# Kernel optimization log

Measured on AMD Instinct MI355X. Metric: run time of the kernel, lower is better.

Reference implementation:

```python
import jax, jax.numpy as jnp
import numpy as np

WS = 8          # window_size
NH = 8          # num_heads
IQKV = 128      # inner_qk_v_dim
IQKC = 32       # inner_qk_c_dim
IVV = 64        # inner_v_v_dim
EPS = 1e-6
B, HH, WW, DV, DC = 2, 224, 224, 256, 64


def _rmsnorm(x, g):
    return x * jax.lax.rsqrt(jnp.mean(x * x, axis=-1, keepdims=True) + EPS) * g


def _window(x):
    # (b, h, w, d) -> (b, Wh, Ww, ws*ws, d)
    b, h, w, d = x.shape
    x = x.reshape(b, h // WS, WS, w // WS, WS, d).transpose(0, 1, 3, 2, 4, 5)
    return x.reshape(b, h // WS, w // WS, WS * WS, d)


def _unwindow(x, h, w):
    # (b, N, ws*ws, d) -> (b, h, w, d)
    b, _, _, d = x.shape
    x = x.reshape(b, h // WS, w // WS, WS, WS, d).transpose(0, 1, 3, 2, 4, 5)
    return x.reshape(b, h, w, d)


def _source_qkv(V, C, Wqk_v, bqk_v, g_v, Wqk_c, bqk_c, g_c, Wv):
    Vw, Cw = _window(V), _window(C)          # (b, Wh, Ww, n, d)
    b, Wh, Ww, n, _ = Vw.shape
    N = Wh * Ww
    Vavg, Cavg = Vw.mean(-2), Cw.mean(-2)
    qk_v = _rmsnorm(Vavg @ Wqk_v + bqk_v, g_v)   # (b, Wh, Ww, 2*IQKV)
    qk_c = _rmsnorm(Cavg @ Wqk_c + bqk_c, g_c)   # (b, Wh, Ww, 2*IQKC)
    # 'b Wh Ww (H e) -> b H (Wh Ww) e' then chunk2 along e
    qk_v = qk_v.reshape(b, N, NH, -1).transpose(0, 2, 1, 3)
    qk_c = qk_c.reshape(b, N, NH, -1).transpose(0, 2, 1, 3)
    ev, ec = qk_v.shape[-1] // 2, qk_c.shape[-1] // 2
    qv, kv = qk_v[..., :ev], qk_v[..., ev:]
    qc, kc = qk_c[..., :ec], qk_c[..., ec:]
    # value projection: 'b Wh Ww n (e H) -> b H (Wh Ww) (n e)'
    e = IVV // NH
    Vv = (Vw @ Wv).reshape(b, N, n, e, NH).transpose(0, 4, 1, 2, 3).reshape(b, NH, N, n * e)
    return qv, kv, qc, kc, Vv, (Wh, Ww)


def _forward(values0, coords0, values1, coords1,
             Wqk_v, bqk_v, g_v, Wqk_c, bqk_c, g_c, Wv, Wback):
    parts = [_source_qkv(V, C, Wqk_v, bqk_v, g_v, Wqk_c, bqk_c, g_c, Wv)
             for V, C in ((values0, coords0), (values1, coords1))]
    qv = jnp.concatenate([p[0] for p in parts], axis=2)
    kv = jnp.concatenate([p[1] for p in parts], axis=2)
    qc = jnp.concatenate([p[2] for p in parts], axis=2)
    kc = jnp.concatenate([p[3] for p in parts], axis=2)
    Vv = jnp.concatenate([p[4] for p in parts], axis=2)
    scores = (jnp.einsum('bhqe,bhke->bhqk', qv, kv) / jnp.sqrt(jnp.float32(IQKV))
              + jnp.einsum('bhqe,bhke->bhqk', qc, kc) / jnp.sqrt(jnp.float32(IQKC)))
    A = jax.nn.softmax(scores, axis=-1)            # (b, H, N, N)
    rw = jnp.einsum('bhqk,bhkf->bhqf', A, Vv)      # (b, H, N, n*e)
    b, _, N, _ = rw.shape
    n, e = WS * WS, IVV // NH
    # 'b H N (n e) -> b N n (e H)'
    rw = rw.reshape(b, NH, N, n, e).transpose(0, 2, 3, 4, 1).reshape(b, N, n, e * NH)
    rw = rw @ Wback                                # (b, N, n, Dv)
    outs, off = [], 0
    for (V, _), p in zip(((values0, coords0), (values1, coords1)), parts):
        Wh, Ww = p[5]
        Ns = Wh * Ww
        outs.append(_unwindow(rw[:, off:off + Ns], Wh * WS, Ww * WS))
        off += Ns
    return tuple(outs)


def setup_inputs() -> dict:
    key = jax.random.key(0)
    ks = jax.random.split(key, 8)
    s = 0.02
    return {
        'values0': jax.random.normal(ks[0], (B, HH, WW, DV), jnp.float32),
        'coords0': jax.random.normal(ks[1], (B, HH, WW, DC), jnp.float32),
        'values1': jax.random.normal(ks[2], (B, HH, WW, DV), jnp.float32),
        'coords1': jax.random.normal(ks[3], (B, HH, WW, DC), jnp.float32),
        'Wqk_v': s * jax.random.normal(ks[4], (DV, 2 * IQKV), jnp.float32),
        'bqk_v': jnp.zeros((2 * IQKV,), jnp.float32),
        'g_v': jnp.ones((2 * IQKV,), jnp.float32),
        'Wqk_c': s * jax.random.normal(ks[5], (DC, 2 * IQKC), jnp.float32),
        'bqk_c': jnp.zeros((2 * IQKC,), jnp.float32),
        'g_c': jnp.ones((2 * IQKC,), jnp.float32),
        'Wv': s * jax.random.normal(ks[6], (DV, IVV), jnp.float32),
        'Wback': s * jax.random.normal(ks[7], (IVV, DV), jnp.float32),
    }


def reference(values0, coords0, values1, coords1,
              Wqk_v, bqk_v, g_v, Wqk_c, bqk_c, g_c, Wv, Wback):
    return _forward(values0, coords0, values1, coords1,
                    Wqk_v, bqk_v, g_v, Wqk_c, bqk_c, g_c, Wv, Wback)
```

## Files before the change

### kernel.cpp

```cpp
#include <hip/hip_runtime.h>

#define NSRC 784
#define NTOT 1568
#define NHD 8
#define DVC 256
#define DCC 64
#define D20 20
#define FDIM 512
#define OUT_PER_SRC 25690112

typedef short s16x8 __attribute__((ext_vector_type(8)));
typedef unsigned short u16x8 __attribute__((ext_vector_type(8)));
typedef float f32x4 __attribute__((ext_vector_type(4)));
typedef float f32x16 __attribute__((ext_vector_type(16)));
typedef unsigned u32x4 __attribute__((ext_vector_type(4)));

__device__ __forceinline__ unsigned short f2bf(float x) {
    unsigned u = __float_as_uint(x);
    unsigned r = (u + 0x7FFFu + ((u >> 16) & 1u)) >> 16;
    return (unsigned short)r;
}

__device__ __forceinline__ unsigned cvt_pk_bf16(float lo, float hi) {
    unsigned r;
    asm volatile("v_cvt_pk_bf16_f32 %0, %1, %2" : "=v"(r) : "v"(lo), "v"(hi));
    return r;
}

__device__ __forceinline__ void split_bf(float x, unsigned short& hi, unsigned short& lo) {
    unsigned short h = f2bf(x);
    float hf = __uint_as_float(((unsigned)h) << 16);
    hi = h;
    lo = f2bf(x - hf);
}

__global__ __launch_bounds__(256) void kz_zero(unsigned short* __restrict__ p) {
    size_t i = (size_t)blockIdx.x * 256 + threadIdx.x;
    u16x8 z = (u16x8)0;
    *(u16x8*)&p[i * 8] = z;
}

__global__ __launch_bounds__(256) void k0_wsplit(
    const float* __restrict__ Wv,
    unsigned short* __restrict__ WThi, unsigned short* __restrict__ WTlo) {
    int e = blockIdx.x, dd = threadIdx.x;
    float x = Wv[dd * DCC + e];
    unsigned short h, l;
    split_bf(x, h, l);
    WThi[e * 256 + dd] = h;
    WTlo[e * 256 + dd] = l;
}

__global__ __launch_bounds__(256) void k0b_wback(
    const float* __restrict__ Wb, unsigned short* __restrict__ Wp) {
    int idx = blockIdx.x * 256 + threadIdx.x;
    int jj = idx & 7, lane = (idx >> 3) & 63, hl = (idx >> 9) & 1;
    int kc = (idx >> 10) & 1, mt = idx >> 11;
    int c = mt * 16 + (lane & 15);
    int j = kc * 32 + (lane >> 4) * 8 + jj;
    unsigned short h, l;
    split_bf(Wb[j * 256 + c], h, l);
    Wp[idx] = hl ? l : h;
}

__global__ __launch_bounds__(256) void k1c_avg(
    const float* __restrict__ c0, const float* __restrict__ c1,
    float* __restrict__ Cavg) {
    int wi = blockIdx.x * 4 + (threadIdx.x >> 6);
    int d = threadIdx.x & 63;
    int b = wi / NTOT, N = wi % NTOT;
    int src = N / NSRC, nloc = N % NSRC;
    int wh = nloc / 28, ww = nloc % 28;
    const float* __restrict__ C = src ? c1 : c0;
    int pbase = (b * 224 + wh * 8) * 224 + ww * 8;
    float s = 0.f;
#pragma unroll 8
    for (int p = 0; p < 64; ++p)
        s += C[(size_t)(pbase + (p >> 3) * 224 + (p & 7)) * DCC + d];
    Cavg[(size_t)wi * DCC + d] = s * 0.015625f;
}

__global__ __launch_bounds__(256) void k2_qk(
    const float* __restrict__ Vavg, const float* __restrict__ Cavg,
    const float* __restrict__ Wqkv, const float* __restrict__ bqkv, const float* __restrict__ gv,
    const float* __restrict__ Wqkc, const float* __restrict__ bqkc, const float* __restrict__ gc,
    unsigned short* __restrict__ Qp, unsigned short* __restrict__ Kp) {
    __shared__ float xv[DVC];
    __shared__ float xc[DCC];
    __shared__ float wred[4];
    int blk = blockIdx.x;
    int b = blk / NTOT, N = blk % NTOT;
    int t = threadIdx.x;
    int tile = N >> 5, l31 = N & 31;
    xv[t] = Vavg[(size_t)blk * DVC + t];
    if (t < DCC) xc[t] = Cavg[(size_t)blk * DCC + t];
    __syncthreads();
    float yv = bqkv[t];
#pragma unroll 4
    for (int d = 0; d < DVC; ++d) yv += xv[d] * Wqkv[d * 256 + t];
    float ss = yv * yv;
#pragma unroll
    for (int off = 32; off; off >>= 1) ss += __shfl_xor(ss, off, 64);
    if ((t & 63) == 0) wred[t >> 6] = ss;
    __syncthreads();
    float tot = wred[0] + wred[1] + wred[2] + wred[3];
    float rv = rsqrtf(tot * (1.f / 256.f) + 1e-6f);
    float yn = yv * rv * gv[t];
    int h = t >> 5, c = t & 31;
    int bh = b * NHD + h;
    {
        int isq = (c < 16);
        int d = isq ? c : c - 16;
        float val = isq ? yn * 0.088388347648318447f : yn;
        unsigned short h16, l16;
        split_bf(val, h16, l16);
        int hh = d >> 3, j = d & 7;
        size_t base = ((size_t)(bh * 49 + tile) * 4) * 512 + (size_t)(hh * 32 + l31) * 8 + j;
        unsigned short* dst = isq ? Qp : Kp;
        dst[base] = h16;
        dst[base + 1024] = l16;
    }
    if (t < DCC) {
        float yc = bqkc[t];
#pragma unroll 4
        for (int d = 0; d < DCC; ++d) yc += xc[d] * Wqkc[d * 64 + t];
        float sc = yc * yc;
#pragma unroll
        for (int off = 32; off; off >>= 1) sc += __shfl_xor(sc, off, 64);
        float rc = rsqrtf(sc * (1.f / 64.f) + 1e-6f);
        float ycn = yc * rc * gc[t];
        int h2 = t >> 3, c2 = t & 7;
        int bh2 = b * NHD + h2;
        int isq = (c2 < 4);
        int dd = isq ? c2 : c2 - 4;
        float val = isq ? ycn * 0.17677669529663687f : ycn;
        unsigned short h16, l16;
        split_bf(val, h16, l16);
        size_t base = ((size_t)(bh2 * 49 + tile) * 4 + 1) * 512 + (size_t)l31 * 8 + dd;
        unsigned short* dst = isq ? Qp : Kp;
        dst[base] = h16;
        dst[base + 1024] = l16;
    }
}

__global__ __launch_bounds__(256) void k3_vv(
    const float* __restrict__ v0, const float* __restrict__ v1,
    const unsigned short* __restrict__ WThi, const unsigned short* __restrict__ WTlo,
    unsigned short* __restrict__ Vvb, float* __restrict__ Vavg) {
    __shared__ unsigned short Ahi[64 * 40];
    __shared__ unsigned short Alo[64 * 40];
    __shared__ float avgpart[256];
    __shared__ float avgrow[256];
    int blk = blockIdx.x;
    int b = blk / NTOT, N = blk % NTOT;
    int src = N / NSRC, nloc = N % NSRC;
    int wh = nloc / 28, ww = nloc % 28;
    const float* __restrict__ V = src ? v1 : v0;
    int t = threadIdx.x;
    int w = t >> 6, lane = t & 63;
    int lm = lane & 15, lk = lane >> 4;
    int ddl = t & 31;
    int pg = t >> 5;
    int pbase = (b * 224 + wh * 8) * 224 + ww * 8;
    const float* xptr[8];
#pragma unroll
    for (int i = 0; i < 8; ++i) {
        int px = i * 8 + pg;
        xptr[i] = V + (size_t)(pbase + (px >> 3) * 224 + (px & 7)) * DVC + ddl;
    }
    f32x4 acc4[4];
#pragma unroll
    for (int nt = 0; nt < 4; ++nt) acc4[nt] = (f32x4)0.f;

    for (int c = 0; c < 8; ++c) {
        int d0 = c * 32;
        float xs[8];
#pragma unroll
        for (int i = 0; i < 8; ++i) xs[i] = xptr[i][d0];
        float part = 0.f;
#pragma unroll
        for (int i = 0; i < 8; ++i) part += xs[i];
        __syncthreads();
        avgpart[t] = part;
#pragma unroll
        for (int i = 0; i < 8; ++i) {
            int px = i * 8 + pg;
            unsigned short h, l;
            split_bf(xs[i], h, l);
            Ahi[px * 40 + ddl] = h;
            Alo[px * 40 + ddl] = l;
        }
        __syncthreads();
        if (t < 32) {
            float s = 0.f;
#pragma unroll
            for (int g = 0; g < 8; ++g) s += avgpart[g * 32 + t];
            avgrow[d0 + t] = s * 0.015625f;
        }
        s16x8 ahi = *(const s16x8*)&Ahi[(w * 16 + lm) * 40 + lk * 8];
        s16x8 alo = *(const s16x8*)&Alo[(w * 16 + lm) * 40 + lk * 8];
#pragma unroll
        for (int nt = 0; nt < 4; ++nt) {
            int e = nt * 16 + lm;
            s16x8 bhi = *(const s16x8*)&WThi[e * 256 + d0 + lk * 8];
            s16x8 blo = *(const s16x8*)&WTlo[e * 256 + d0 + lk * 8];
            acc4[nt] = __builtin_amdgcn_mfma_f32_16x16x32_bf16(ahi, blo, acc4[nt], 0, 0, 0);
            acc4[nt] = __builtin_amdgcn_mfma_f32_16x16x32_bf16(alo, bhi, acc4[nt], 0, 0, 0);
            acc4[nt] = __builtin_amdgcn_mfma_f32_16x16x32_bf16(ahi, bhi, acc4[nt], 0, 0, 0);
        }
    }
#pragma unroll
    for (int nt = 0; nt < 4; ++nt) {
        int e = nt * 16 + lm;
#pragma unroll
        for (int r = 0; r < 4; ++r) {
            int px = w * 16 + lk * 4 + r;
            Vvb[((size_t)(b * NHD + (e & 7)) * NTOT + N) * FDIM + px * 8 + (e >> 3)] = f2bf(acc4[nt][r]);
        }
    }
    __syncthreads();
    Vavg[(size_t)blk * DVC + t] = avgrow[t];
}

__global__ __launch_bounds__(256) void k3b_pack(
    const unsigned short* __restrict__ Vvb, unsigned short* __restrict__ Vp) {
    __shared__ unsigned short tile[32 * 520];
    int kt = blockIdx.x, bh = blockIdx.y;
    int t = threadIdx.x;
    const unsigned short* src = Vvb + ((size_t)bh * NTOT + kt * 32) * FDIM;
#pragma unroll
    for (int it = 0; it < 8; ++it) {
        int flat = it * 256 + t;
        int r = flat >> 6, c8 = (flat & 63) * 8;
        *(u16x8*)&tile[r * 520 + c8] = *(const u16x8*)&src[(size_t)r * FDIM + c8];
    }
    __syncthreads();
    unsigned short* dst = Vp + ((size_t)bh * 49 + kt) * 16384;
#pragma unroll
    for (int it = 0; it < 8; ++it) {
        int flato = it * 256 + t;
        int lane = flato & 63;
        int kh = (flato >> 6) & 1;
        int sub = (flato >> 7) & 3;
        int w = flato >> 9;
        int l31 = lane & 31, hh = lane >> 5;
        int f = w * 128 + sub * 32 + l31;
        int kbase = kh * 16 + hh * 8;
        u16x8 v;
#pragma unroll
        for (int j = 0; j < 8; ++j) v[j] = tile[(kbase + j) * 520 + f];
        *(u16x8*)&dst[(size_t)flato * 8] = v;
    }
}

__global__ __launch_bounds__(256) void k4_attn(
    const unsigned short* __restrict__ Qp, const unsigned short* __restrict__ Kp,
    const unsigned short* __restrict__ Vp, float* __restrict__ rw) {
    __shared__ float ebuf[32 * 132];
    int wg = blockIdx.x;
    int qt = wg >> 4, bh = wg & 15;
    int q0 = qt * 32;
    int t = threadIdx.x;
    int w = t >> 6, lane = t & 63;
    int l31 = lane & 31, hh = lane >> 5;

    const unsigned short* __restrict__ Qpb = Qp + ((size_t)(bh * 49 + qt) * 4) * 512 + lane * 8;
    const unsigned short* __restrict__ Kpb = Kp + (size_t)bh * 49 * 2048 + lane * 8;
    const unsigned short* __restrict__ Vpb = Vp + (size_t)bh * 49 * 16384 + lane * 8;

    s16x8 qa0 = *(const s16x8*)&Qpb[0];
    s16x8 qa1 = *(const s16x8*)&Qpb[512];
    s16x8 ql0 = *(const s16x8*)&Qpb[1024];
    s16x8 ql1 = *(const s16x8*)&Qpb[1536];

    s16x8 ka0 = *(const s16x8*)&Kpb[0];
    s16x8 ka1 = *(const s16x8*)&Kpb[512];
    s16x8 kl0 = *(const s16x8*)&Kpb[1024];
    s16x8 kl1 = *(const s16x8*)&Kpb[1536];

    float m = -1e30f, lsum = 0.f;
    f32x16 acc[4];
#pragma unroll
    for (int s = 0; s < 4; ++s) acc[s] = (f32x16)0.f;

    for (int kt = 0; kt < NTOT / 32; ++kt) {
        const unsigned short* Vtile = Vpb + (size_t)kt * 16384 + (w * 8) * 512;
        s16x8 va[8];
#pragma unroll
        for (int fr = 0; fr < 8; ++fr)
            va[fr] = *(const s16x8*)&Vtile[fr * 512];
        int ktn = (kt < 48) ? kt + 1 : 48;
        const unsigned short* Ktn = Kpb + (size_t)ktn * 2048;
        s16x8 kn0 = *(const s16x8*)&Ktn[0];
        s16x8 kn1 = *(const s16x8*)&Ktn[512];
        s16x8 kn2 = *(const s16x8*)&Ktn[1024];
        s16x8 kn3 = *(const s16x8*)&Ktn[1536];

        f32x16 sacc = (f32x16)0.f;
        sacc = __builtin_amdgcn_mfma_f32_32x32x16_bf16(kl0, qa0, sacc, 0, 0, 0);
        sacc = __builtin_amdgcn_mfma_f32_32x32x16_bf16(ka0, ql0, sacc, 0, 0, 0);
        sacc = __builtin_amdgcn_mfma_f32_32x32x16_bf16(ka0, qa0, sacc, 0, 0, 0);
        sacc = __builtin_amdgcn_mfma_f32_32x32x16_bf16(kl1, qa1, sacc, 0, 0, 0);
        sacc = __builtin_amdgcn_mfma_f32_32x32x16_bf16(ka1, ql1, sacc, 0, 0, 0);
        sacc = __builtin_amdgcn_mfma_f32_32x32x16_bf16(ka1, qa1, sacc, 0, 0, 0);

        float tmax = sacc[0];
#pragma unroll
        for (int r = 1; r < 16; ++r) tmax = fmaxf(tmax, sacc[r]);
        tmax = fmaxf(tmax, __shfl_xor(tmax, 32, 64));
        if (__any(tmax > m + 8.f)) {
            float mn = fmaxf(m, tmax);
            float sc = __expf(m - mn);
#pragma unroll
            for (int s = 0; s < 4; ++s) acc[s] = acc[s] * sc;
            lsum *= sc;
            m = mn;
        }
        unsigned P2[8];
        float tsum = 0.f;
#pragma unroll
        for (int j = 0; j < 8; ++j) {
            float pa = __expf(sacc[2 * j] - m);
            float pb = __expf(sacc[2 * j + 1] - m);
            tsum += pa + pb;
            P2[j] = cvt_pk_bf16(pa, pb);
        }
        lsum += tsum + __shfl_xor(tsum, 32, 64);
        unsigned X2[8];
#pragma unroll
        for (int j = 0; j < 8; ++j) X2[j] = (unsigned)__shfl_xor((int)P2[j], 32, 64);
        u32x4 b0u, b1u;
        if (hh == 0) {
            b0u[0] = P2[0]; b0u[1] = P2[1]; b0u[2] = X2[0]; b0u[3] = X2[1];
            b1u[0] = P2[4]; b1u[1] = P2[5]; b1u[2] = X2[4]; b1u[3] = X2[5];
        } else {
            b0u[0] = X2[2]; b0u[1] = X2[3]; b0u[2] = P2[2]; b0u[3] = P2[3];
            b1u[0] = X2[6]; b1u[1] = X2[7]; b1u[2] = P2[6]; b1u[3] = P2[7];
        }
        s16x8 pb0 = __builtin_bit_cast(s16x8, b0u);
        s16x8 pb1 = __builtin_bit_cast(s16x8, b1u);

#pragma unroll
        for (int sub = 0; sub < 4; ++sub) {
            acc[sub] = __builtin_amdgcn_mfma_f32_32x32x16_bf16(va[2 * sub],     pb0, acc[sub], 0, 0, 0);
            acc[sub] = __builtin_amdgcn_mfma_f32_32x32x16_bf16(va[2 * sub + 1], pb1, acc[sub], 0, 0, 0);
        }
        ka0 = kn0; ka1 = kn1; kl0 = kn2; kl1 = kn3;
    }

    float inv = 1.f / lsum;
    float* rwg = rw + ((size_t)bh * NTOT + q0) * FDIM;
#pragma unroll
    for (int c = 0; c < 4; ++c) {
        __syncthreads();
        if (w == c) {
#pragma unroll
            for (int sub = 0; sub < 4; ++sub) {
#pragma unroll
                for (int r = 0; r < 16; ++r) {
                    int fl = sub * 32 + (r & 3) + 8 * (r >> 2) + 4 * hh;
                    ebuf[l31 * 132 + fl] = acc[sub][r] * inv;
                }
            }
        }
        __syncthreads();
        int qr = t >> 3, cb = (t & 7) * 16;
#pragma unroll
        for (int j = 0; j < 4; ++j) {
            *(float4*)&rwg[(size_t)qr * FDIM + c * 128 + cb + j * 4] =
                *(const float4*)&ebuf[qr * 132 + cb + j * 4];
        }
    }
}

__global__ __launch_bounds__(256) void k5_back(
    const float* __restrict__ rw, const unsigned short* __restrict__ Wp,
    float* __restrict__ out) {
    __shared__ unsigned short SB[2 * 64 * 72];
    unsigned short* BhL = SB;
    unsigned short* BlL = SB + 64 * 72;
    int blk = blockIdx.x;
    int b = blk / NTOT, N = blk % NTOT;
    int src = N / NSRC, nloc = N % NSRC;
    int wh = nloc / 28, ww = nloc % 28;
    int t = threadIdx.x;
    int w = t >> 6, lane = t & 63;
    int lm = lane & 15, lk = lane >> 4;
    int pbase = (b * 224 + wh * 8) * 224 + ww * 8;

#pragma unroll
    for (int i = 0; i < 4; ++i) {
        int flat4 = i * 256 + t;
        int h = flat4 >> 7;
        int f0 = (flat4 & 127) * 4;
        float4 v = *(const float4*)&rw[((size_t)(b * NHD + h) * NTOT + N) * FDIM + f0];
        int n = f0 >> 3;
        int ebase = f0 & 7;
        float vv[4] = {v.x, v.y, v.z, v.w};
#pragma unroll
        for (int u = 0; u < 4; ++u) {
            int j8 = ebase + u;
            unsigned short h16, l16;
            split_bf(vv[u], h16, l16);
            int col = ((j8 ^ (n & 7)) << 3) | h;
            BhL[n * 72 + col] = h16;
            BlL[n * 72 + col] = l16;
        }
    }
    __syncthreads();

    f32x4 acc[4][4];
#pragma unroll
    for (int mi = 0; mi < 4; ++mi)
#pragma unroll
        for (int nt = 0; nt < 4; ++nt) acc[mi][nt] = (f32x4)0.f;

    const unsigned short* Wpw = Wp + (size_t)(w * 4) * 2048 + lane * 8;
#pragma unroll
    for (int kc = 0; kc < 2; ++kc) {
        s16x8 Ah[4], Al[4], Bh4[4], Bl4[4];
#pragma unroll
        for (int mi = 0; mi < 4; ++mi) {
            int base = mi * 2048 + kc * 1024;
            Ah[mi] = *(const s16x8*)&Wpw[base];
            Al[mi] = *(const s16x8*)&Wpw[base + 512];
        }
#pragma unroll
        for (int nt = 0; nt < 4; ++nt) {
            int n = nt * 16 + lm;
            int addr = n * 72 + (((kc * 4 + lk) ^ (n & 7)) << 3);
            Bh4[nt] = *(const s16x8*)&BhL[addr];
            Bl4[nt] = *(const s16x8*)&BlL[addr];
        }
#pragma unroll
        for (int mi = 0; mi < 4; ++mi)
#pragma unroll
            for (int nt = 0; nt < 4; ++nt) {
                acc[mi][nt] = __builtin_amdgcn_mfma_f32_16x16x32_bf16(Ah[mi], Bl4[nt], acc[mi][nt], 0, 0, 0);
                acc[mi][nt] = __builtin_amdgcn_mfma_f32_16x16x32_bf16(Al[mi], Bh4[nt], acc[mi][nt], 0, 0, 0);
                acc[mi][nt] = __builtin_amdgcn_mfma_f32_16x16x32_bf16(Ah[mi], Bh4[nt], acc[mi][nt], 0, 0, 0);
            }
    }

    float* eb = (float*)SB;
    float* outp = out + (size_t)src * OUT_PER_SRC;
#pragma unroll
    for (int ch = 0; ch < 4; ++ch) {
        __syncthreads();
        if (w == ch) {
#pragma unroll
            for (int mi = 0; mi < 4; ++mi)
#pragma unroll
                for (int nt = 0; nt < 4; ++nt)
#pragma unroll
                    for (int r = 0; r < 4; ++r) {
                        int n = nt * 16 + lm;
                        int cl = mi * 16 + lk * 4 + r;
                        eb[n * 68 + cl] = acc[mi][nt][r];
                    }
        }
        __syncthreads();
#pragma unroll
        for (int i = 0; i < 4; ++i) {
            int fl4 = i * 256 + t;
            int n = fl4 >> 4, c4 = (fl4 & 15) * 4;
            int opix = pbase + (n >> 3) * 224 + (n & 7);
            *(float4*)&outp[(size_t)opix * DVC + ch * 64 + c4] =
                *(const float4*)&eb[n * 68 + c4];
        }
    }
}

extern "C" void kernel_launch(void* const* d_in, const int* in_sizes, int n_in,
                              void* d_out, int out_size, void* d_ws, size_t ws_size,
                              hipStream_t stream) {
    const float* v0   = (const float*)d_in[0];
    const float* c0   = (const float*)d_in[1];
    const float* v1   = (const float*)d_in[2];
    const float* c1   = (const float*)d_in[3];
    const float* Wqkv = (const float*)d_in[4];
    const float* bqkv = (const float*)d_in[5];
    const float* gv   = (const float*)d_in[6];
    const float* Wqkc = (const float*)d_in[7];
    const float* bqkc = (const float*)d_in[8];
    const float* gc   = (const float*)d_in[9];
    const float* Wv   = (const float*)d_in[10];
    const float* Wbk  = (const float*)d_in[11];

    float* ws = (float*)d_ws;
    float* rw   = ws;
    float* Vavg = ws;
    float* Cavg = ws + 802816;
    unsigned short* Qp   = (unsigned short*)(ws + 12845056);
    unsigned short* Kp   = (unsigned short*)(ws + 13647872);
    unsigned short* WThi = (unsigned short*)(ws + 14450688);
    unsigned short* WTlo = (unsigned short*)(ws + 14458880);
    unsigned short* Vvb  = (unsigned short*)(ws + 14467072);
    unsigned short* Vp   = (unsigned short*)(ws + 20889600);
    unsigned short* Wp   = (unsigned short*)(ws + 27312128);

    float* outp = (float*)d_out;

    kz_zero  <<<1568, 256, 0, stream>>>(Qp);
    k0_wsplit<<<64, 256, 0, stream>>>(Wv, WThi, WTlo);
    k0b_wback<<<256, 256, 0, stream>>>(Wbk, Wp);
    k3_vv    <<<2 * NTOT, 256, 0, stream>>>(v0, v1, WThi, WTlo, Vvb, Vavg);
    k1c_avg  <<<784, 256, 0, stream>>>(c0, c1, Cavg);
    k2_qk    <<<2 * NTOT, 256, 0, stream>>>(Vavg, Cavg, Wqkv, bqkv, gv, Wqkc, bqkc, gc, Qp, Kp);
    k3b_pack <<<dim3(49, 16), 256, 0, stream>>>(Vvb, Vp);
    k4_attn  <<<784, 256, 0, stream>>>(Qp, Kp, Vp, rw);
    k5_back  <<<2 * NTOT, 256, 0, stream>>>(rw, Wp, outp);
}
```

Baseline: 391.4 us.

## Restructure k3_vv loads into float4 two-phase tiles with register-held window averages

The value-projection kernel now loads window pixels as float4 vectors in two 128-channel phases instead of eight scalar 32-channel chunks, so there are fewer global load instructions and block barriers. Each wave loads only its own 16 pixels. Window-average partial sums stay in registers and are reduced once at the end through a lane shuffle and shared memory, replacing the per-chunk shared-memory reduction. The shared staging buffers grow to 128 columns, which raises LDS use per block and may lower occupancy.

```diff
diff --git a/kernel.cpp b/kernel.cpp
--- a/kernel.cpp
+++ b/kernel.cpp
@@ -11,6 +11,7 @@
 
 typedef short s16x8 __attribute__((ext_vector_type(8)));
 typedef unsigned short u16x8 __attribute__((ext_vector_type(8)));
+typedef unsigned short u16x4 __attribute__((ext_vector_type(4)));
 typedef float f32x4 __attribute__((ext_vector_type(4)));
 typedef float f32x16 __attribute__((ext_vector_type(16)));
 typedef unsigned u32x4 __attribute__((ext_vector_type(4)));
@@ -147,10 +148,8 @@
     const float* __restrict__ v0, const float* __restrict__ v1,
     const unsigned short* __restrict__ WThi, const unsigned short* __restrict__ WTlo,
     unsigned short* __restrict__ Vvb, float* __restrict__ Vavg) {
-    __shared__ unsigned short Ahi[64 * 40];
-    __shared__ unsigned short Alo[64 * 40];
-    __shared__ float avgpart[256];
-    __shared__ float avgrow[256];
+    __shared__ unsigned short Ahi[64 * 138];
+    __shared__ unsigned short Alo[64 * 138];
     int blk = blockIdx.x;
     int b = blk / NTOT, N = blk % NTOT;
     int src = N / NSRC, nloc = N % NSRC;
@@ -159,54 +158,58 @@
     int t = threadIdx.x;
     int w = t >> 6, lane = t & 63;
     int lm = lane & 15, lk = lane >> 4;
-    int ddl = t & 31;
-    int pg = t >> 5;
+    int pxw = w * 16;
+    int lhalf = lane >> 5;
+    int d4 = (lane & 31) * 4;
     int pbase = (b * 224 + wh * 8) * 224 + ww * 8;
-    const float* xptr[8];
-#pragma unroll
-    for (int i = 0; i < 8; ++i) {
-        int px = i * 8 + pg;
-        xptr[i] = V + (size_t)(pbase + (px >> 3) * 224 + (px & 7)) * DVC + ddl;
-    }
+
+    float ap[8] = {0.f, 0.f, 0.f, 0.f, 0.f, 0.f, 0.f, 0.f};
     f32x4 acc4[4];
 #pragma unroll
     for (int nt = 0; nt < 4; ++nt) acc4[nt] = (f32x4)0.f;
 
-    for (int c = 0; c < 8; ++c) {
-        int d0 = c * 32;
-        float xs[8];
-#pragma unroll
-        for (int i = 0; i < 8; ++i) xs[i] = xptr[i][d0];
-        float part = 0.f;
-#pragma unroll
-        for (int i = 0; i < 8; ++i) part += xs[i];
+#pragma unroll
+    for (int ph = 0; ph < 2; ++ph) {
+        int d0 = ph * 128;
+        float4 xs[8];
+#pragma unroll
+        for (int i = 0; i < 8; ++i) {
+            int px = pxw + i * 2 + lhalf;
+            xs[i] = *(const float4*)&V[(size_t)(pbase + (px >> 3) * 224 + (px & 7)) * DVC + d0 + d4];
+        }
+#pragma unroll
+        for (int i = 0; i < 8; ++i) {
+            ap[ph * 4 + 0] += xs[i].x; ap[ph * 4 + 1] += xs[i].y;
+            ap[ph * 4 + 2] += xs[i].z; ap[ph * 4 + 3] += xs[i].w;
+        }
+        if (ph) __syncthreads();
+#pragma unroll
+        for (int i = 0; i < 8; ++i) {
+            int px = pxw + i * 2 + lhalf;
+            u16x4 h4, l4;
+            unsigned short hq, lq;
+            split_bf(xs[i].x, hq, lq); h4[0] = hq; l4[0] = lq;
+            split_bf(xs[i].y, hq, lq); h4[1] = hq; l4[1] = lq;
+            split_bf(xs[i].z, hq, lq); h4[2] = hq; l4[2] = lq;
+            split_bf(xs[i].w, hq, lq); h4[3] = hq; l4[3] = lq;
+            *(u16x4*)&Ahi[px * 138 + d4] = h4;
+            *(u16x4*)&Alo[px * 138 + d4] = l4;
+        }
         __syncthreads();
-        avgpart[t] = part;
-#pragma unroll
-        for (int i = 0; i < 8; ++i) {
-            int px = i * 8 + pg;
-            unsigned short h, l;
-            split_bf(xs[i], h, l);
-            Ahi[px * 40 + ddl] = h;
-            Alo[px * 40 + ddl] = l;
-        }
-        __syncthreads();
-        if (t < 32) {
-            float s = 0.f;
-#pragma unroll
-            for (int g = 0; g < 8; ++g) s += avgpart[g * 32 + t];
-            avgrow[d0 + t] = s * 0.015625f;
-        }
-        s16x8 ahi = *(const s16x8*)&Ahi[(w * 16 + lm) * 40 + lk * 8];
-        s16x8 alo = *(const s16x8*)&Alo[(w * 16 + lm) * 40 + lk * 8];
-#pragma unroll
-        for (int nt = 0; nt < 4; ++nt) {
-            int e = nt * 16 + lm;
-            s16x8 bhi = *(const s16x8*)&WThi[e * 256 + d0 + lk * 8];
-            s16x8 blo = *(const s16x8*)&WTlo[e * 256 + d0 + lk * 8];
-            acc4[nt] = __builtin_amdgcn_mfma_f32_16x16x32_bf16(ahi, blo, acc4[nt], 0, 0, 0);
-            acc4[nt] = __builtin_amdgcn_mfma_f32_16x16x32_bf16(alo, bhi, acc4[nt], 0, 0, 0);
-            acc4[nt] = __builtin_amdgcn_mfma_f32_16x16x32_bf16(ahi, bhi, acc4[nt], 0, 0, 0);
+#pragma unroll
+        for (int c2 = 0; c2 < 4; ++c2) {
+            int dd0 = c2 * 32;
+            s16x8 ahi = *(const s16x8*)&Ahi[(pxw + lm) * 138 + dd0 + lk * 8];
+            s16x8 alo = *(const s16x8*)&Alo[(pxw + lm) * 138 + dd0 + lk * 8];
+#pragma unroll
+            for (int nt = 0; nt < 4; ++nt) {
+                int e = nt * 16 + lm;
+                s16x8 bhi = *(const s16x8*)&WThi[e * 256 + d0 + dd0 + lk * 8];
+                s16x8 blo = *(const s16x8*)&WTlo[e * 256 + d0 + dd0 + lk * 8];
+                acc4[nt] = __builtin_amdgcn_mfma_f32_16x16x32_bf16(ahi, blo, acc4[nt], 0, 0, 0);
+                acc4[nt] = __builtin_amdgcn_mfma_f32_16x16x32_bf16(alo, bhi, acc4[nt], 0, 0, 0);
+                acc4[nt] = __builtin_amdgcn_mfma_f32_16x16x32_bf16(ahi, bhi, acc4[nt], 0, 0, 0);
+            }
         }
     }
 #pragma unroll
@@ -218,8 +221,20 @@
             Vvb[((size_t)(b * NHD + (e & 7)) * NTOT + N) * FDIM + px * 8 + (e >> 3)] = f2bf(acc4[nt][r]);
         }
     }
+#pragma unroll
+    for (int j = 0; j < 8; ++j) ap[j] += __shfl_xor(ap[j], 32, 64);
     __syncthreads();
-    Vavg[(size_t)blk * DVC + t] = avgrow[t];
+    float* avgb = (float*)Ahi;
+    if (lhalf == 0) {
+#pragma unroll
+        for (int ph = 0; ph < 2; ++ph) {
+            float4 v4 = make_float4(ap[ph * 4], ap[ph * 4 + 1], ap[ph * 4 + 2], ap[ph * 4 + 3]);
+            *(float4*)&avgb[w * 256 + ph * 128 + d4] = v4;
+        }
+    }
+    __syncthreads();
+    Vavg[(size_t)blk * DVC + t] =
+        (avgb[t] + avgb[256 + t] + avgb[512 + t] + avgb[768 + t]) * 0.015625f;
 }
 
 __global__ __launch_bounds__(256) void k3b_pack(
```

Result: no change. 389.9 us (-0.4%).
